# Kernel optimization log

Measured on AMD Instinct MI355X. Metric: run time of the kernel, lower is better.

## Reference

```python
import jax, jax.numpy as jnp
import numpy as np

# Single-device reference: with head-parallel world size 1, both _SeqAllToAll
# collectives are identities, so the forward is exactly the kv-packed causal
# attention computed by loongtrain_attn_kvpacked_func (flash-attn semantics).

def setup_inputs() -> dict:
    key = jax.random.key(0)
    k1, k2 = jax.random.split(key)
    B, S, H, D = 1, 2048, 32, 128
    q = jax.random.normal(k1, (B, S, H, D), dtype=jnp.float32)
    kv = jax.random.normal(k2, (B, S, 2, H, D), dtype=jnp.float32)
    return {"q": q, "kv": kv}


def reference(q, kv) -> jnp.ndarray:
    # q: [B, S, H, D]; kv: [B, S, 2, H, D] (flash-attn kvpacked layout)
    B, S, H, D = q.shape
    k = kv[:, :, 0]  # [B, S, H, D]
    v = kv[:, :, 1]  # [B, S, H, D]
    scale = 1.0 / jnp.sqrt(jnp.asarray(D, dtype=q.dtype))
    # scores: [B, H, Sq, Sk]
    scores = jnp.einsum("bshd,bthd->bhst", q, k) * scale
    # causal mask (LoongTrain attention is causal)
    causal = jnp.tril(jnp.ones((S, S), dtype=bool))
    scores = jnp.where(causal[None, None, :, :], scores, jnp.asarray(-jnp.inf, dtype=scores.dtype))
    probs = jax.nn.softmax(scores, axis=-1)
    # context: [B, S, H, D]
    context = jnp.einsum("bhst,bthd->bshd", probs, v)
    return context
```

## Files before the change

kernel.cpp:

```cpp
#include <hip/hip_runtime.h>
#include <hip/hip_bf16.h>

typedef __bf16 bf16_t;
typedef __bf16 bf16x4 __attribute__((ext_vector_type(4)));
typedef __bf16 bf16x8 __attribute__((ext_vector_type(8)));
typedef float  f32x4  __attribute__((ext_vector_type(4)));

constexpr int S  = 2048;
constexpr int H  = 32;
constexpr int D  = 128;
constexpr int BR = 128;
constexpr int SC = 32;
constexpr int NT = S / BR;
constexpr int KSTR  = 136;
constexpr int VSTR2 = 20;
constexpr int PSTR  = 40;

__device__ __forceinline__ bf16x8 cvt8(f32x4 lo, f32x4 hi) {
    bf16x8 r;
#pragma unroll
    for (int j = 0; j < 4; ++j) { r[j] = (bf16_t)lo[j]; r[4 + j] = (bf16_t)hi[j]; }
    return r;
}
__device__ __forceinline__ uint32_t pk2(float a, float b) {
    union { uint32_t u; bf16_t h[2]; } r;
    r.h[0] = (bf16_t)a; r.h[1] = (bf16_t)b;
    return r.u;
}

__global__ __launch_bounds__(256, 1)
void fa_fwd(const float* __restrict__ q, const float* __restrict__ kvp,
            float* __restrict__ out) {
    __shared__ __align__(16) bf16_t   Klds[2][SC * KSTR];
    __shared__ __align__(16) uint32_t Vt2[2][D * VSTR2];
    __shared__ __align__(16) bf16_t   PT[4 * 32 * PSTR];

    const int bx = blockIdx.x;
    const int h  = bx & 31;
    const int pr = bx >> 5;

    const int t    = threadIdx.x;
    const int w    = t >> 6;
    const int lane = t & 63;
    const int quad = lane >> 4;
    const int m    = lane & 15;

    const float sc = 0.08838834764831845f * 1.44269504088896340f;

    const int k2 = t >> 4, kc = t & 15;
    const size_t rowstep = (size_t)2 * H * D;
    const size_t tstep   = (size_t)SC * rowstep;
    const float* pkbase = kvp + (((size_t)(2 * k2) * 2 + 0) * H + h) * D + kc * 8;
    const float* pvbase = kvp + (((size_t)(2 * k2) * 2 + 1) * H + h) * D + kc * 8;
    const int vpos = k2 ^ ((kc & 3) << 2);
    bf16_t* PTw = &PT[w * 32 * PSTR];

    f32x4 kr[2][2], vr[2][2];

    for (int phase = 0; phase < 2; ++phase) {
        const int qtile = phase ? (NT - 1 - pr) : pr;
        const int q0    = qtile * BR;
        const int qp0   = q0 + w * 32 + m;
        const int nkv   = (qtile + 1) * (BR / SC);
        const int qmaxw = q0 + w * 32 + 31;

        bf16x8 aq[2][4];
#pragma unroll
        for (int g = 0; g < 2; ++g)
#pragma unroll
            for (int c = 0; c < 4; ++c) {
                const float* p = q + ((size_t)(qp0 + g * 16) * H + h) * D + c * 32 + quad * 8;
                f32x4 lo = *(const f32x4*)p * sc;
                f32x4 hi = *(const f32x4*)(p + 4) * sc;
                aq[g][c] = cvt8(lo, hi);
            }

        f32x4 o[2][8];
#pragma unroll
        for (int g = 0; g < 2; ++g)
#pragma unroll
            for (int i = 0; i < 8; ++i) o[g][i] = (f32x4)0.f;
        float lrow[2] = {0.f, 0.f};

        const float* pk = pkbase;
        const float* pv = pvbase;

        auto ldregs = [&]() {
            kr[0][0] = *(const f32x4*)pk;             kr[0][1] = *(const f32x4*)(pk + 4);
            kr[1][0] = *(const f32x4*)(pk + rowstep); kr[1][1] = *(const f32x4*)(pk + rowstep + 4);
            vr[0][0] = *(const f32x4*)pv;             vr[0][1] = *(const f32x4*)(pv + 4);
            vr[1][0] = *(const f32x4*)(pv + rowstep); vr[1][1] = *(const f32x4*)(pv + rowstep + 4);
        };
        auto stage = [&](int b) {
            *(bf16x8*)&Klds[b][(2 * k2)     * KSTR + kc * 8] = cvt8(kr[0][0], kr[0][1]);
            *(bf16x8*)&Klds[b][(2 * k2 + 1) * KSTR + kc * 8] = cvt8(kr[1][0], kr[1][1]);
#pragma unroll
            for (int j = 0; j < 8; ++j) {
                const int d = kc * 8 + j;
                const float a = (j < 4) ? vr[0][0][j] : vr[0][1][j - 4];
                const float bb = (j < 4) ? vr[1][0][j] : vr[1][1][j - 4];
                Vt2[b][d * VSTR2 + vpos] = pk2(a, bb);
            }
        };

        ldregs();
        stage(0);
        if (nkv > 1) { pk += tstep; pv += tstep; ldregs(); }
        __syncthreads();

        for (int kb = 0; kb < nkv; ++kb) {
            const int kv0 = kb * SC;
            const int cur = kb & 1;

            if (kb + 1 < nkv) {
                stage(cur ^ 1);
                if (kb + 2 < nkv) { pk += tstep; pv += tstep; ldregs(); }
            }

            if (kv0 <= qmaxw) {
                f32x4 sA[2][2];
#pragma unroll
                for (int g = 0; g < 2; ++g) { sA[g][0] = (f32x4)0.f; sA[g][1] = (f32x4)0.f; }
#pragma unroll
                for (int c = 0; c < 4; ++c) {
                    bf16x8 ak0 = *(const bf16x8*)&Klds[cur][m * KSTR + c * 32 + quad * 8];
                    bf16x8 ak1 = *(const bf16x8*)&Klds[cur][(16 + m) * KSTR + c * 32 + quad * 8];
                    sA[0][0] = __builtin_amdgcn_mfma_f32_16x16x32_bf16(ak0, aq[0][c], sA[0][0], 0, 0, 0);
                    sA[0][1] = __builtin_amdgcn_mfma_f32_16x16x32_bf16(ak1, aq[0][c], sA[0][1], 0, 0, 0);
                    sA[1][0] = __builtin_amdgcn_mfma_f32_16x16x32_bf16(ak0, aq[1][c], sA[1][0], 0, 0, 0);
                    sA[1][1] = __builtin_amdgcn_mfma_f32_16x16x32_bf16(ak1, aq[1][c], sA[1][1], 0, 0, 0);
                }

#pragma unroll
                for (int g = 0; g < 2; ++g) {
                    const int lim = (qp0 + g * 16) - kv0;
                    float p[8], rs = 0.f;
#pragma unroll
                    for (int r = 0; r < 4; ++r) {
                        float e0 = __builtin_amdgcn_exp2f(fminf(sA[g][0][r], 80.f));
                        float e1 = __builtin_amdgcn_exp2f(fminf(sA[g][1][r], 80.f));
                        p[r]     = (quad * 4 + r      <= lim) ? e0 : 0.f;
                        p[4 + r] = (16 + quad * 4 + r <= lim) ? e1 : 0.f;
                        rs += p[r] + p[4 + r];
                    }
                    bf16x4 pa, pb;
#pragma unroll
                    for (int r = 0; r < 4; ++r) { pa[r] = (bf16_t)p[r]; pb[r] = (bf16_t)p[4 + r]; }
                    *(bf16x4*)&PTw[(g * 16 + m) * PSTR + quad * 4]      = pa;
                    *(bf16x4*)&PTw[(g * 16 + m) * PSTR + 16 + quad * 4] = pb;
                    rs += __shfl_xor(rs, 16);
                    rs += __shfl_xor(rs, 32);
                    lrow[g] += rs;
                }
                asm volatile("s_waitcnt lgkmcnt(0)" ::: "memory");
                bf16x8 bp0 = *(const bf16x8*)&PTw[m * PSTR + quad * 8];
                bf16x8 bp1 = *(const bf16x8*)&PTw[(16 + m) * PSTR + quad * 8];

#pragma unroll
                for (int tt = 0; tt < 8; ++tt) {
                    const int dd  = tt * 16 + m;
                    const int grp = quad ^ ((dd >> 3) & 3);
                    bf16x8 av = *(const bf16x8*)&Vt2[cur][dd * VSTR2 + grp * 4];
                    o[0][tt] = __builtin_amdgcn_mfma_f32_16x16x32_bf16(av, bp0, o[0][tt], 0, 0, 0);
                    o[1][tt] = __builtin_amdgcn_mfma_f32_16x16x32_bf16(av, bp1, o[1][tt], 0, 0, 0);
                }
            }
            __syncthreads();
        }

#pragma unroll
        for (int g = 0; g < 2; ++g) {
            const float inv = 1.0f / lrow[g];
            float* op = out + ((size_t)(qp0 + g * 16) * H + h) * D;
#pragma unroll
            for (int tt = 0; tt < 8; ++tt) {
                f32x4 val = o[g][tt] * inv;
                *(f32x4*)(op + tt * 16 + quad * 4) = val;
            }
        }
    }
}

extern "C" void kernel_launch(void* const* d_in, const int* in_sizes, int n_in,
                              void* d_out, int out_size, void* d_ws, size_t ws_size,
                              hipStream_t stream) {
    const float* q  = (const float*)d_in[0];
    const float* kv = (const float*)d_in[1];
    float* out = (float*)d_out;
    dim3 grid(H * (NT / 2));
    dim3 block(256);
    fa_fwd<<<grid, block, 0, stream>>>(q, kv, out);
}
```

Baseline: 203.2 us.

## Launch one block per q-tile with longest-first ordering and 2 blocks/CU

Replaces the paired-tile two-phase loop with one block per (q-tile, head). Tiles are ordered so the longest causal tiles launch first, and launch bounds now allow two blocks per CU for more occupancy. The loop body is reordered so the QK MMA, softmax and V loads happen before staging the next K/V tile, which overlaps global loads with compute. The row-sum shuffles are deferred to the end. More blocks adds per-block Q load and prologue overhead, and tighter register limits could cause spills.

```diff
diff --git a/kernel.cpp b/kernel.cpp
--- a/kernel.cpp
+++ b/kernel.cpp
@@ -28,7 +28,7 @@
     return r.u;
 }
 
-__global__ __launch_bounds__(256, 1)
+__global__ __launch_bounds__(256, 2)
 void fa_fwd(const float* __restrict__ q, const float* __restrict__ kvp,
             float* __restrict__ out) {
     __shared__ __align__(16) bf16_t   Klds[2][SC * KSTR];
@@ -37,7 +37,9 @@
 
     const int bx = blockIdx.x;
     const int h  = bx & 31;
-    const int pr = bx >> 5;
+    const int i  = bx >> 5;
+    const int qtile = (i < 8) ? (15 - i) : (i - 8);
+    const int q0    = qtile * BR;
 
     const int t    = threadIdx.x;
     const int w    = t >> 6;
@@ -50,133 +52,136 @@
     const int k2 = t >> 4, kc = t & 15;
     const size_t rowstep = (size_t)2 * H * D;
     const size_t tstep   = (size_t)SC * rowstep;
-    const float* pkbase = kvp + (((size_t)(2 * k2) * 2 + 0) * H + h) * D + kc * 8;
-    const float* pvbase = kvp + (((size_t)(2 * k2) * 2 + 1) * H + h) * D + kc * 8;
+    const float* pk = kvp + (((size_t)(2 * k2) * 2 + 0) * H + h) * D + kc * 8;
+    const float* pv = kvp + (((size_t)(2 * k2) * 2 + 1) * H + h) * D + kc * 8;
     const int vpos = k2 ^ ((kc & 3) << 2);
     bf16_t* PTw = &PT[w * 32 * PSTR];
 
+    const int qp0   = q0 + w * 32 + m;
+    const int nkv   = (qtile + 1) * (BR / SC);
+    const int qmaxw = q0 + w * 32 + 31;
+
+    bf16x8 aq[2][4];
+#pragma unroll
+    for (int g = 0; g < 2; ++g)
+#pragma unroll
+        for (int c = 0; c < 4; ++c) {
+            const float* p = q + ((size_t)(qp0 + g * 16) * H + h) * D + c * 32 + quad * 8;
+            f32x4 lo = *(const f32x4*)p * sc;
+            f32x4 hi = *(const f32x4*)(p + 4) * sc;
+            aq[g][c] = cvt8(lo, hi);
+        }
+
+    f32x4 o[2][8];
+#pragma unroll
+    for (int g = 0; g < 2; ++g)
+#pragma unroll
+        for (int idx = 0; idx < 8; ++idx) o[g][idx] = (f32x4)0.f;
+    float lrow[2] = {0.f, 0.f};
+
     f32x4 kr[2][2], vr[2][2];
+    auto ldregs = [&]() {
+        kr[0][0] = *(const f32x4*)pk;             kr[0][1] = *(const f32x4*)(pk + 4);
+        kr[1][0] = *(const f32x4*)(pk + rowstep); kr[1][1] = *(const f32x4*)(pk + rowstep + 4);
+        vr[0][0] = *(const f32x4*)pv;             vr[0][1] = *(const f32x4*)(pv + 4);
+        vr[1][0] = *(const f32x4*)(pv + rowstep); vr[1][1] = *(const f32x4*)(pv + rowstep + 4);
+    };
+    auto stage = [&](int b) {
+        *(bf16x8*)&Klds[b][(2 * k2)     * KSTR + kc * 8] = cvt8(kr[0][0], kr[0][1]);
+        *(bf16x8*)&Klds[b][(2 * k2 + 1) * KSTR + kc * 8] = cvt8(kr[1][0], kr[1][1]);
+#pragma unroll
+        for (int j = 0; j < 8; ++j) {
+            const int d = kc * 8 + j;
+            const float a  = (j < 4) ? vr[0][0][j] : vr[0][1][j - 4];
+            const float bb = (j < 4) ? vr[1][0][j] : vr[1][1][j - 4];
+            Vt2[b][d * VSTR2 + vpos] = pk2(a, bb);
+        }
+    };
 
-    for (int phase = 0; phase < 2; ++phase) {
-        const int qtile = phase ? (NT - 1 - pr) : pr;
-        const int q0    = qtile * BR;
-        const int qp0   = q0 + w * 32 + m;
-        const int nkv   = (qtile + 1) * (BR / SC);
-        const int qmaxw = q0 + w * 32 + 31;
+    ldregs();
+    stage(0);
+    if (nkv > 1) { pk += tstep; pv += tstep; ldregs(); }
+    __syncthreads();
 
-        bf16x8 aq[2][4];
+    for (int kb = 0; kb < nkv; ++kb) {
+        const int kv0 = kb * SC;
+        const int cur = kb & 1;
+        const bool active = (kv0 <= qmaxw);
+
+        bf16x8 bp0, bp1, av[8];
+        if (active) {
+            f32x4 sA[2][2];
 #pragma unroll
-        for (int g = 0; g < 2; ++g)
+            for (int g = 0; g < 2; ++g) { sA[g][0] = (f32x4)0.f; sA[g][1] = (f32x4)0.f; }
 #pragma unroll
             for (int c = 0; c < 4; ++c) {
-                const float* p = q + ((size_t)(qp0 + g * 16) * H + h) * D + c * 32 + quad * 8;
-                f32x4 lo = *(const f32x4*)p * sc;
-                f32x4 hi = *(const f32x4*)(p + 4) * sc;
-                aq[g][c] = cvt8(lo, hi);
+                bf16x8 ak0 = *(const bf16x8*)&Klds[cur][m * KSTR + c * 32 + quad * 8];
+                bf16x8 ak1 = *(const bf16x8*)&Klds[cur][(16 + m) * KSTR + c * 32 + quad * 8];
+                sA[0][0] = __builtin_amdgcn_mfma_f32_16x16x32_bf16(ak0, aq[0][c], sA[0][0], 0, 0, 0);
+                sA[0][1] = __builtin_amdgcn_mfma_f32_16x16x32_bf16(ak1, aq[0][c], sA[0][1], 0, 0, 0);
+                sA[1][0] = __builtin_amdgcn_mfma_f32_16x16x32_bf16(ak0, aq[1][c], sA[1][0], 0, 0, 0);
+                sA[1][1] = __builtin_amdgcn_mfma_f32_16x16x32_bf16(ak1, aq[1][c], sA[1][1], 0, 0, 0);
             }
 
-        f32x4 o[2][8];
 #pragma unroll
-        for (int g = 0; g < 2; ++g)
+            for (int g = 0; g < 2; ++g) {
+                const int lim = (qp0 + g * 16) - kv0;
+                float p[8], rs = 0.f;
 #pragma unroll
-            for (int i = 0; i < 8; ++i) o[g][i] = (f32x4)0.f;
-        float lrow[2] = {0.f, 0.f};
+                for (int r = 0; r < 4; ++r) {
+                    float e0 = __builtin_amdgcn_exp2f(fminf(sA[g][0][r], 80.f));
+                    float e1 = __builtin_amdgcn_exp2f(fminf(sA[g][1][r], 80.f));
+                    p[r]     = (quad * 4 + r      <= lim) ? e0 : 0.f;
+                    p[4 + r] = (16 + quad * 4 + r <= lim) ? e1 : 0.f;
+                    rs += p[r] + p[4 + r];
+                }
+                lrow[g] += rs;
+                bf16x4 pa, pb;
+#pragma unroll
+                for (int r = 0; r < 4; ++r) { pa[r] = (bf16_t)p[r]; pb[r] = (bf16_t)p[4 + r]; }
+                *(bf16x4*)&PTw[(g * 16 + m) * PSTR + quad * 4]      = pa;
+                *(bf16x4*)&PTw[(g * 16 + m) * PSTR + 16 + quad * 4] = pb;
+            }
+            asm volatile("s_waitcnt lgkmcnt(0)" ::: "memory");
+            bp0 = *(const bf16x8*)&PTw[m * PSTR + quad * 8];
+            bp1 = *(const bf16x8*)&PTw[(16 + m) * PSTR + quad * 8];
+#pragma unroll
+            for (int tt = 0; tt < 8; ++tt) {
+                const int dd  = tt * 16 + m;
+                const int grp = quad ^ ((dd >> 3) & 3);
+                av[tt] = *(const bf16x8*)&Vt2[cur][dd * VSTR2 + grp * 4];
+            }
+        }
 
-        const float* pk = pkbase;
-        const float* pv = pvbase;
+        if (kb + 1 < nkv) {
+            stage(cur ^ 1);
+            if (kb + 2 < nkv) { pk += tstep; pv += tstep; ldregs(); }
+        }
 
-        auto ldregs = [&]() {
-            kr[0][0] = *(const f32x4*)pk;             kr[0][1] = *(const f32x4*)(pk + 4);
-            kr[1][0] = *(const f32x4*)(pk + rowstep); kr[1][1] = *(const f32x4*)(pk + rowstep + 4);
-            vr[0][0] = *(const f32x4*)pv;             vr[0][1] = *(const f32x4*)(pv + 4);
-            vr[1][0] = *(const f32x4*)(pv + rowstep); vr[1][1] = *(const f32x4*)(pv + rowstep + 4);
-        };
-        auto stage = [&](int b) {
-            *(bf16x8*)&Klds[b][(2 * k2)     * KSTR + kc * 8] = cvt8(kr[0][0], kr[0][1]);
-            *(bf16x8*)&Klds[b][(2 * k2 + 1) * KSTR + kc * 8] = cvt8(kr[1][0], kr[1][1]);
+        if (active) {
 #pragma unroll
-            for (int j = 0; j < 8; ++j) {
-                const int d = kc * 8 + j;
-                const float a = (j < 4) ? vr[0][0][j] : vr[0][1][j - 4];
-                const float bb = (j < 4) ? vr[1][0][j] : vr[1][1][j - 4];
-                Vt2[b][d * VSTR2 + vpos] = pk2(a, bb);
+            for (int tt = 0; tt < 8; ++tt) {
+                o[0][tt] = __builtin_amdgcn_mfma_f32_16x16x32_bf16(av[tt], bp0, o[0][tt], 0, 0, 0);
+                o[1][tt] = __builtin_amdgcn_mfma_f32_16x16x32_bf16(av[tt], bp1, o[1][tt], 0, 0, 0);
             }
-        };
-
-        ldregs();
-        stage(0);
-        if (nkv > 1) { pk += tstep; pv += tstep; ldregs(); }
+        }
         __syncthreads();
-
-        for (int kb = 0; kb < nkv; ++kb) {
-            const int kv0 = kb * SC;
-            const int cur = kb & 1;
-
-            if (kb + 1 < nkv) {
-                stage(cur ^ 1);
-                if (kb + 2 < nkv) { pk += tstep; pv += tstep; ldregs(); }
-            }
-
-            if (kv0 <= qmaxw) {
-                f32x4 sA[2][2];
-#pragma unroll
-                for (int g = 0; g < 2; ++g) { sA[g][0] = (f32x4)0.f; sA[g][1] = (f32x4)0.f; }
-#pragma unroll
-                for (int c = 0; c < 4; ++c) {
-                    bf16x8 ak0 = *(const bf16x8*)&Klds[cur][m * KSTR + c * 32 + quad * 8];
-                    bf16x8 ak1 = *(const bf16x8*)&Klds[cur][(16 + m) * KSTR + c * 32 + quad * 8];
-                    sA[0][0] = __builtin_amdgcn_mfma_f32_16x16x32_bf16(ak0, aq[0][c], sA[0][0], 0, 0, 0);
-                    sA[0][1] = __builtin_amdgcn_mfma_f32_16x16x32_bf16(ak1, aq[0][c], sA[0][1], 0, 0, 0);
-                    sA[1][0] = __builtin_amdgcn_mfma_f32_16x16x32_bf16(ak0, aq[1][c], sA[1][0], 0, 0, 0);
-                    sA[1][1] = __builtin_amdgcn_mfma_f32_16x16x32_bf16(ak1, aq[1][c], sA[1][1], 0, 0, 0);
-                }
+    }
 
 #pragma unroll
-                for (int g = 0; g < 2; ++g) {
-                    const int lim = (qp0 + g * 16) - kv0;
-                    float p[8], rs = 0.f;
-#pragma unroll
-                    for (int r = 0; r < 4; ++r) {
-                        float e0 = __builtin_amdgcn_exp2f(fminf(sA[g][0][r], 80.f));
-                        float e1 = __builtin_amdgcn_exp2f(fminf(sA[g][1][r], 80.f));
-                        p[r]     = (quad * 4 + r      <= lim) ? e0 : 0.f;
-                        p[4 + r] = (16 + quad * 4 + r <= lim) ? e1 : 0.f;
-                        rs += p[r] + p[4 + r];
-                    }
-                    bf16x4 pa, pb;
-#pragma unroll
-                    for (int r = 0; r < 4; ++r) { pa[r] = (bf16_t)p[r]; pb[r] = (bf16_t)p[4 + r]; }
-                    *(bf16x4*)&PTw[(g * 16 + m) * PSTR + quad * 4]      = pa;
-                    *(bf16x4*)&PTw[(g * 16 + m) * PSTR + 16 + quad * 4] = pb;
-                    rs += __shfl_xor(rs, 16);
-                    rs += __shfl_xor(rs, 32);
-                    lrow[g] += rs;
-                }
-                asm volatile("s_waitcnt lgkmcnt(0)" ::: "memory");
-                bf16x8 bp0 = *(const bf16x8*)&PTw[m * PSTR + quad * 8];
-                bf16x8 bp1 = *(const bf16x8*)&PTw[(16 + m) * PSTR + quad * 8];
+    for (int g = 0; g < 2; ++g) {
+        lrow[g] += __shfl_xor(lrow[g], 16);
+        lrow[g] += __shfl_xor(lrow[g], 32);
+    }
 
 #pragma unroll
-                for (int tt = 0; tt < 8; ++tt) {
-                    const int dd  = tt * 16 + m;
-                    const int grp = quad ^ ((dd >> 3) & 3);
-                    bf16x8 av = *(const bf16x8*)&Vt2[cur][dd * VSTR2 + grp * 4];
-                    o[0][tt] = __builtin_amdgcn_mfma_f32_16x16x32_bf16(av, bp0, o[0][tt], 0, 0, 0);
-                    o[1][tt] = __builtin_amdgcn_mfma_f32_16x16x32_bf16(av, bp1, o[1][tt], 0, 0, 0);
-                }
-            }
-            __syncthreads();
-        }
-
+    for (int g = 0; g < 2; ++g) {
+        const float inv = 1.0f / lrow[g];
+        float* op = out + ((size_t)(qp0 + g * 16) * H + h) * D;
 #pragma unroll
-        for (int g = 0; g < 2; ++g) {
-            const float inv = 1.0f / lrow[g];
-            float* op = out + ((size_t)(qp0 + g * 16) * H + h) * D;
-#pragma unroll
-            for (int tt = 0; tt < 8; ++tt) {
-                f32x4 val = o[g][tt] * inv;
-                *(f32x4*)(op + tt * 16 + quad * 4) = val;
-            }
+        for (int tt = 0; tt < 8; ++tt) {
+            f32x4 val = o[g][tt] * inv;
+            *(f32x4*)(op + tt * 16 + quad * 4) = val;
         }
     }
 }
@@ -187,7 +192,7 @@
     const float* q  = (const float*)d_in[0];
     const float* kv = (const float*)d_in[1];
     float* out = (float*)d_out;
-    dim3 grid(H * (NT / 2));
+    dim3 grid(NT * H);
     dim3 block(256);
     fa_fwd<<<grid, block, 0, stream>>>(q, kv, out);
 }
```

New measurement: 180.9 us. 11.0% less time.
